# Performance work log

Measured on AMD Instinct MI355X. Metric: run time of the kernel, lower is better.

## Reference

```python
import jax, jax.numpy as jnp
import numpy as np

TEMP = 0.07
HARD_K = 512
EMB_D = 768
PROJ_D = 128
QUEUE = 32768
BATCH = 2048
NUM_CLASSES = 2


def setup_inputs() -> dict:
    key = jax.random.key(0)
    ks = jax.random.split(key, 8)
    embeddings = jax.random.normal(ks[0], (BATCH, EMB_D), dtype=jnp.float32)
    labels = jax.random.randint(ks[1], (BATCH,), 0, NUM_CLASSES)
    # projector params: Linear(D,D) -> ReLU -> Linear(D,128)
    W1 = jax.random.normal(ks[2], (EMB_D, EMB_D), dtype=jnp.float32) * 0.02
    b1 = jnp.zeros((EMB_D,), dtype=jnp.float32)
    W2 = jax.random.normal(ks[3], (EMB_D, PROJ_D), dtype=jnp.float32) * 0.02
    b2 = jnp.zeros((PROJ_D,), dtype=jnp.float32)
    # queue buffers: L2-normalized random embeddings (as in __init__) with valid labels
    qe = jax.random.normal(ks[4], (QUEUE, PROJ_D), dtype=jnp.float32)
    queue_embeddings = qe / jnp.linalg.norm(qe, axis=1, keepdims=True)
    queue_labels = jax.random.randint(ks[5], (QUEUE,), 0, NUM_CLASSES)
    return {
        'embeddings': embeddings, 'labels': labels,
        'W1': W1, 'b1': b1, 'W2': W2, 'b2': b2,
        'queue_embeddings': queue_embeddings, 'queue_labels': queue_labels,
    }


def reference(embeddings, labels, W1, b1, W2, b2, queue_embeddings, queue_labels):
    n = embeddings.shape[0]
    # projector + L2 normalize
    h = jax.nn.relu(embeddings @ W1 + b1)
    z = h @ W2 + b2
    z = z / jnp.linalg.norm(z, axis=1, keepdims=True)  # (N, 128)

    # pairwise in-batch similarities, scaled by temperature
    S = (z @ z.T) / TEMP  # (N, N)
    same = labels[:, None] == labels[None, :]
    eye = jnp.eye(n, dtype=bool)
    pos_mask = same & ~eye           # positives: same label, not self
    neg_mask = ~same                 # in-batch negatives: different label

    # logsumexp over in-batch negatives per anchor (-inf rows -> -inf, handled by logaddexp)
    neg_batch = jnp.where(neg_mask, S, -jnp.inf)
    lse_batch = jax.scipy.special.logsumexp(neg_batch, axis=1)  # (N,)

    # hard negatives from queue: opposite-label, top-K by similarity
    sims_q = z @ queue_embeddings.T  # (N, Q)
    opp = (queue_labels[None, :] != labels[:, None]) & (queue_labels[None, :] >= 0)
    masked_q = jnp.where(opp, sims_q, -jnp.inf)
    topk_vals, _ = jax.lax.top_k(masked_q, HARD_K)  # (N, K); -inf pads drop from logsumexp
    # fallback (no opposite-label entries): first K queue embeddings regardless of label
    fallback = sims_q[:, :HARD_K]
    has_opp = opp.any(axis=1, keepdims=True)
    neg_q = jnp.where(has_opp, topk_vals, fallback) / TEMP
    lse_queue = jax.scipy.special.logsumexp(neg_q, axis=1)  # (N,)

    # all negatives for anchor i: batch negatives ++ queue hard negatives
    lse_neg = jnp.logaddexp(lse_batch, lse_queue)  # (N,)

    # per positive pair (i, j): log_prob = pos_sim - logsumexp([pos_sim, negs])
    log_prob = S - jnp.logaddexp(S, lse_neg[:, None])  # (N, N)
    losses = jnp.where(pos_mask, -log_prob, 0.0)
    count = pos_mask.sum()
    return jnp.where(count > 0, losses.sum() / count.astype(losses.dtype), 0.0)
```

## Files before the change

### kernel.cpp

```cpp
#include <hip/hip_runtime.h>
#include <hip/hip_fp16.h>

#define BATCH_N   2048
#define EMB_D_    768
#define PROJ_D_   128
#define QUEUE_N   32768
#define HARD_K_   512
static constexpr float INV_T  = 1.0f / 0.07f;
static constexpr float WLO    = 0.12f;
static constexpr float S8ENC  = 255.0f / 0.88f;
static constexpr float BINW   = 0.88f / 255.0f;

typedef __attribute__((ext_vector_type(8))) short short8;
typedef __attribute__((ext_vector_type(4))) short short4v;
typedef __attribute__((ext_vector_type(4))) float f32x4;

__device__ __forceinline__ unsigned short f2bf(float f) {
    unsigned u = __float_as_uint(f);
    unsigned r = u + 0x7fffu + ((u >> 16) & 1u);
    return (unsigned short)(r >> 16);
}
__device__ __forceinline__ float bf2f(short s) {
    return __uint_as_float(((unsigned)(unsigned short)s) << 16);
}
__device__ __forceinline__ int opp_of(int mylab, const int* __restrict__ qcnt) {
    const int same = (mylab == 0) ? qcnt[0] : ((mylab == 1) ? qcnt[1] : 0);
    return qcnt[2] - same;
}

__global__ void __launch_bounds__(256) mfma_s_pack(const short* __restrict__ Ab,
                                                   const short* __restrict__ Bb,
                                                   short* __restrict__ C, int N) {
    __shared__ __align__(16) short As[128 * 128];
    __shared__ __align__(16) short Bs[128 * 128];
    const int t = threadIdx.x;
    const int lane = t & 63, wv = t >> 6;
    const int l16 = lane & 15, l4 = lane >> 4;
    const int m0 = blockIdx.y * 128, n0 = blockIdx.x * 128;

    #pragma unroll
    for (int it = 0; it < 8; ++it) {
        const int r = it * 4 + wv, row = r * 4 + l4, cg = l16 ^ (row & 15);
        __builtin_amdgcn_global_load_lds(
            (const __attribute__((address_space(1))) void*)(Ab + (size_t)(m0 + row) * 128 + cg * 8),
            (__attribute__((address_space(3))) void*)(As + r * 512), 16, 0, 0);
    }
    #pragma unroll
    for (int it = 0; it < 8; ++it) {
        const int r = it * 4 + wv, row = r * 4 + l4, cg = l16 ^ (row & 15);
        __builtin_amdgcn_global_load_lds(
            (const __attribute__((address_space(1))) void*)(Bb + (size_t)(n0 + row) * 128 + cg * 8),
            (__attribute__((address_space(3))) void*)(Bs + r * 512), 16, 0, 0);
    }
    __syncthreads();

    const int wm = (wv & 1) * 64, wn = (wv >> 1) * 64;
    f32x4 acc[4][4];
    #pragma unroll
    for (int i = 0; i < 4; ++i)
        #pragma unroll
        for (int j = 0; j < 4; ++j) acc[i][j] = f32x4{0.f, 0.f, 0.f, 0.f};

    #pragma unroll
    for (int ks = 0; ks < 4; ++ks) {
        short8 af[4], bfr[4];
        const int ch = (ks * 4 + l4) ^ l16;
        #pragma unroll
        for (int i = 0; i < 4; ++i) {
            af[i]  = *(const short8*)(As + (wm + i * 16 + l16) * 128 + ch * 8);
            bfr[i] = *(const short8*)(Bs + (wn + i * 16 + l16) * 128 + ch * 8);
        }
        #pragma unroll
        for (int i = 0; i < 4; ++i)
            #pragma unroll
            for (int j = 0; j < 4; ++j)
                acc[i][j] = __builtin_amdgcn_mfma_f32_16x16x32_bf16(af[i], bfr[j], acc[i][j], 0, 0, 0);
    }
    #pragma unroll
    for (int i = 0; i < 4; ++i)
        #pragma unroll
        for (int r = 0; r < 4; ++r) {
            const int m = m0 + wm + i * 16 + l4 * 4 + r;
            union { unsigned short u[4]; uint2 d; } pk;
            #pragma unroll
            for (int j = 0; j < 4; ++j) pk.u[j] = f2bf(acc[i][j][r]);
            *(uint2*)(C + (size_t)m * N + n0 + wn + l16 * 4) = pk.d;
        }
}

__global__ void __launch_bounds__(256) mfma_mask8(const short* __restrict__ Ab,
                                                  const short* __restrict__ Bb,
                                                  unsigned char* __restrict__ codes,
                                                  const int* __restrict__ labA,
                                                  const int* __restrict__ labB) {
    __shared__ __align__(16) short As[128 * 128];
    __shared__ __align__(16) short Bs[128 * 128];
    const int t = threadIdx.x;
    const int lane = t & 63, wv = t >> 6;
    const int l16 = lane & 15, l4 = lane >> 4;
    const int m0 = blockIdx.y * 128;
    const int wm = (wv & 1) * 64, wn = (wv >> 1) * 64;

    #pragma unroll
    for (int it = 0; it < 8; ++it) {
        const int r = it * 4 + wv, row = r * 4 + l4, cg = l16 ^ (row & 15);
        __builtin_amdgcn_global_load_lds(
            (const __attribute__((address_space(1))) void*)(Ab + (size_t)(m0 + row) * 128 + cg * 8),
            (__attribute__((address_space(3))) void*)(As + r * 512), 16, 0, 0);
    }
    {
        const int n0 = (blockIdx.x * 2) * 128;
        #pragma unroll
        for (int it = 0; it < 8; ++it) {
            const int r = it * 4 + wv, row = r * 4 + l4, cg = l16 ^ (row & 15);
            __builtin_amdgcn_global_load_lds(
                (const __attribute__((address_space(1))) void*)(Bb + (size_t)(n0 + row) * 128 + cg * 8),
                (__attribute__((address_space(3))) void*)(Bs + r * 512), 16, 0, 0);
        }
    }

    int la[16];
    #pragma unroll
    for (int i = 0; i < 4; ++i)
        #pragma unroll
        for (int r = 0; r < 4; ++r)
            la[i * 4 + r] = labA[m0 + wm + i * 16 + l4 * 4 + r];
    const float C0 = 1.0f - WLO * S8ENC;
    __syncthreads();

    #pragma unroll
    for (int tt = 0; tt < 2; ++tt) {
        const int n0 = (blockIdx.x * 2 + tt) * 128;

        f32x4 acc[4][4];
        #pragma unroll
        for (int i = 0; i < 4; ++i)
            #pragma unroll
            for (int j = 0; j < 4; ++j) acc[i][j] = f32x4{0.f, 0.f, 0.f, 0.f};

        #pragma unroll
        for (int ks = 0; ks < 4; ++ks) {
            short8 af[4], bfr[4];
            const int ch = (ks * 4 + l4) ^ l16;
            #pragma unroll
            for (int i = 0; i < 4; ++i) {
                af[i]  = *(const short8*)(As + (wm + i * 16 + l16) * 128 + ch * 8);
                bfr[i] = *(const short8*)(Bs + (wn + i * 16 + l16) * 128 + ch * 8);
            }
            #pragma unroll
            for (int i = 0; i < 4; ++i)
                #pragma unroll
                for (int j = 0; j < 4; ++j)
                    acc[i][j] = __builtin_amdgcn_mfma_f32_16x16x32_bf16(af[i], bfr[j], acc[i][j], 0, 0, 0);
        }

        if (tt == 0) {
            __syncthreads();
            const int n1 = (blockIdx.x * 2 + 1) * 128;
            #pragma unroll
            for (int it = 0; it < 8; ++it) {
                const int r = it * 4 + wv, row = r * 4 + l4, cg = l16 ^ (row & 15);
                __builtin_amdgcn_global_load_lds(
                    (const __attribute__((address_space(1))) void*)(Bb + (size_t)(n1 + row) * 128 + cg * 8),
                    (__attribute__((address_space(3))) void*)(Bs + r * 512), 16, 0, 0);
            }
        }

        float a0[4], a1[4];
        #pragma unroll
        for (int j = 0; j < 4; ++j) {
            const int q = labB[n0 + wn + j * 16 + l16];
            a0[j] = (q >= 0 && q != 0) ? C0 : -1e9f;
            a1[j] = (q >= 0 && q != 1) ? C0 : -1e9f;
        }
        #pragma unroll
        for (int i = 0; i < 4; ++i) {
            #pragma unroll
            for (int r = 0; r < 4; ++r) {
                const int m  = m0 + wm + i * 16 + l4 * 4 + r;
                const bool z = (la[i * 4 + r] == 0);
                unsigned pk = 0;
                #pragma unroll
                for (int j = 0; j < 4; ++j) {
                    const float add = z ? a0[j] : a1[j];
                    const float f = fmaf(acc[i][j][r], S8ENC, add);
#if __has_builtin(__builtin_amdgcn_cvt_pk_u8_f32)
                    pk = __builtin_amdgcn_cvt_pk_u8_f32(f, j, pk);
#else
                    const unsigned c = (unsigned)fminf(fmaxf(f, 0.0f), 255.0f);
                    pk |= c << (8 * j);
#endif
                }
                *(unsigned*)(codes + (size_t)m * QUEUE_N + n0 + wn + l16 * 4) = pk;
            }
        }
        if (tt == 0) __syncthreads();
    }
}

template<typename OutT, bool RELU>
__global__ void __launch_bounds__(256) mfma_nt_k(const short* __restrict__ Ab,
                                                 const short* __restrict__ Bb,
                                                 const float* __restrict__ bias,
                                                 OutT* __restrict__ C,
                                                 int N, int K) {
    __shared__ __align__(16) short As[128 * 128];
    __shared__ __align__(16) short Bs[128 * 128];
    const int t = threadIdx.x;
    const int lane = t & 63, wv = t >> 6;
    const int l16 = lane & 15, l4 = lane >> 4;
    const int m0 = blockIdx.y * 128, n0 = blockIdx.x * 128;
    const int wm = (wv & 1) * 64, wn = (wv >> 1) * 64;

    f32x4 acc[4][4];
    #pragma unroll
    for (int i = 0; i < 4; ++i)
        #pragma unroll
        for (int j = 0; j < 4; ++j) acc[i][j] = f32x4{0.f, 0.f, 0.f, 0.f};

    for (int kb = 0; kb < K; kb += 128) {
        __syncthreads();
        #pragma unroll
        for (int it = 0; it < 8; ++it) {
            const int r = it * 4 + wv, row = r * 4 + l4, cg = l16 ^ (row & 15);
            __builtin_amdgcn_global_load_lds(
                (const __attribute__((address_space(1))) void*)(Ab + (size_t)(m0 + row) * K + kb + cg * 8),
                (__attribute__((address_space(3))) void*)(As + r * 512), 16, 0, 0);
        }
        #pragma unroll
        for (int it = 0; it < 8; ++it) {
            const int r = it * 4 + wv, row = r * 4 + l4, cg = l16 ^ (row & 15);
            __builtin_amdgcn_global_load_lds(
                (const __attribute__((address_space(1))) void*)(Bb + (size_t)(n0 + row) * K + kb + cg * 8),
                (__attribute__((address_space(3))) void*)(Bs + r * 512), 16, 0, 0);
        }
        __syncthreads();
        #pragma unroll
        for (int ks = 0; ks < 4; ++ks) {
            short8 af[4], bfr[4];
            const int ch = (ks * 4 + l4) ^ l16;
            #pragma unroll
            for (int i = 0; i < 4; ++i) {
                af[i]  = *(const short8*)(As + (wm + i * 16 + l16) * 128 + ch * 8);
                bfr[i] = *(const short8*)(Bs + (wn + i * 16 + l16) * 128 + ch * 8);
            }
            #pragma unroll
            for (int i = 0; i < 4; ++i)
                #pragma unroll
                for (int j = 0; j < 4; ++j)
                    acc[i][j] = __builtin_amdgcn_mfma_f32_16x16x32_bf16(af[i], bfr[j], acc[i][j], 0, 0, 0);
        }
    }

    float bsv[4];
    #pragma unroll
    for (int j = 0; j < 4; ++j) bsv[j] = bias[n0 + wn + j * 16 + l16];
    #pragma unroll
    for (int i = 0; i < 4; ++i)
        #pragma unroll
        for (int r = 0; r < 4; ++r) {
            const int m = m0 + wm + i * 16 + l4 * 4 + r;
            #pragma unroll
            for (int j = 0; j < 4; ++j) {
                const int n = n0 + wn + j * 16 + l16;
                float v = acc[i][j][r] + bsv[j];
                if (RELU) v = fmaxf(v, 0.0f);
                if constexpr (sizeof(OutT) == 2) ((short*)C)[(size_t)m * N + n] = (short)f2bf(v);
                else                             ((float*)C)[(size_t)m * N + n] = v;
            }
        }
}

__global__ void __launch_bounds__(256) mfma_z_norm(const short* __restrict__ Ab,
                                                   const short* __restrict__ Bb,
                                                   const float* __restrict__ bias,
                                                   short* __restrict__ zb) {
    __shared__ __align__(16) short As[128 * 128];
    __shared__ __align__(16) short Bs[128 * 128];
    __shared__ float ssq[128];
    const int t = threadIdx.x;
    const int lane = t & 63, wv = t >> 6;
    const int l16 = lane & 15, l4 = lane >> 4;
    const int m0 = blockIdx.x * 128;
    const int wm = (wv & 1) * 64, wn = (wv >> 1) * 64;
    const int K = EMB_D_;

    if (t < 128) ssq[t] = 0.0f;

    f32x4 acc[4][4];
    #pragma unroll
    for (int i = 0; i < 4; ++i)
        #pragma unroll
        for (int j = 0; j < 4; ++j) acc[i][j] = f32x4{0.f, 0.f, 0.f, 0.f};

    for (int kb = 0; kb < K; kb += 128) {
        __syncthreads();
        #pragma unroll
        for (int it = 0; it < 8; ++it) {
            const int r = it * 4 + wv, row = r * 4 + l4, cg = l16 ^ (row & 15);
            __builtin_amdgcn_global_load_lds(
                (const __attribute__((address_space(1))) void*)(Ab + (size_t)(m0 + row) * K + kb + cg * 8),
                (__attribute__((address_space(3))) void*)(As + r * 512), 16, 0, 0);
        }
        #pragma unroll
        for (int it = 0; it < 8; ++it) {
            const int r = it * 4 + wv, row = r * 4 + l4, cg = l16 ^ (row & 15);
            __builtin_amdgcn_global_load_lds(
                (const __attribute__((address_space(1))) void*)(Bb + (size_t)(row) * K + kb + cg * 8),
                (__attribute__((address_space(3))) void*)(Bs + r * 512), 16, 0, 0);
        }
        __syncthreads();
        #pragma unroll
        for (int ks = 0; ks < 4; ++ks) {
            short8 af[4], bfr[4];
            const int ch = (ks * 4 + l4) ^ l16;
            #pragma unroll
            for (int i = 0; i < 4; ++i) {
                af[i]  = *(const short8*)(As + (wm + i * 16 + l16) * 128 + ch * 8);
                bfr[i] = *(const short8*)(Bs + (wn + i * 16 + l16) * 128 + ch * 8);
            }
            #pragma unroll
            for (int i = 0; i < 4; ++i)
                #pragma unroll
                for (int j = 0; j < 4; ++j)
                    acc[i][j] = __builtin_amdgcn_mfma_f32_16x16x32_bf16(af[i], bfr[j], acc[i][j], 0, 0, 0);
        }
    }

    float bsv[4];
    #pragma unroll
    for (int j = 0; j < 4; ++j) bsv[j] = bias[wn + j * 16 + l16];
    #pragma unroll
    for (int i = 0; i < 4; ++i)
        #pragma unroll
        for (int r = 0; r < 4; ++r) {
            float p = 0.0f;
            #pragma unroll
            for (int j = 0; j < 4; ++j) {
                acc[i][j][r] += bsv[j];
                p += acc[i][j][r] * acc[i][j][r];
            }
            #pragma unroll
            for (int o = 8; o > 0; o >>= 1) p += __shfl_xor(p, o);
            if (l16 == 0) atomicAdd(&ssq[wm + i * 16 + l4 * 4 + r], p);
        }
    __syncthreads();
    #pragma unroll
    for (int i = 0; i < 4; ++i)
        #pragma unroll
        for (int r = 0; r < 4; ++r) {
            const int lrow = wm + i * 16 + l4 * 4 + r;
            const float inv = rsqrtf(ssq[lrow]);
            #pragma unroll
            for (int j = 0; j < 4; ++j)
                zb[(size_t)(m0 + lrow) * PROJ_D_ + wn + j * 16 + l16] =
                    (short)f2bf(acc[i][j][r] * inv);
        }
}

__global__ void __launch_bounds__(256) prep(const float* __restrict__ emb, short* __restrict__ embb,
                                            const float* __restrict__ queue, short* __restrict__ qb,
                                            const int* __restrict__ qlab, int* __restrict__ qcnt,
                                            const float* __restrict__ W1, short* __restrict__ w1t,
                                            const float* __restrict__ W2, short* __restrict__ w2t) {
    __shared__ float tile[64][65];
    const int b = blockIdx.x, t = threadIdx.x;
    if (b < 1536) {
        const int i = b * 256 + t;
        const float4 f = ((const float4*)emb)[i];
        short4v o = {(short)f2bf(f.x), (short)f2bf(f.y), (short)f2bf(f.z), (short)f2bf(f.w)};
        ((short4v*)embb)[i] = o;
    } else if (b < 5632) {
        const int i = (b - 1536) * 256 + t;
        const float4 f = ((const float4*)queue)[i];
        short4v o = {(short)f2bf(f.x), (short)f2bf(f.y), (short)f2bf(f.z), (short)f2bf(f.w)};
        ((short4v*)qb)[i] = o;
    } else if (b < 5664) {
        const int i = (b - 5632) * 256 + t;
        int c0 = 0, c1 = 0, cv = 0;
        for (int j = i; j < QUEUE_N; j += 8192) {
            const int q = qlab[j];
            c0 += (q == 0); c1 += (q == 1); cv += (q >= 0);
        }
        #pragma unroll
        for (int o = 32; o > 0; o >>= 1) {
            c0 += __shfl_xor(c0, o); c1 += __shfl_xor(c1, o); cv += __shfl_xor(cv, o);
        }
        if ((t & 63) == 0) {
            atomicAdd(&qcnt[0], c0); atomicAdd(&qcnt[1], c1); atomicAdd(&qcnt[2], cv);
        }
    } else {
        const int bid = b - 5664;
        const float* A; short* At; int R, C, bx, by;
        if (bid < 144) { A = W1; At = w1t; R = EMB_D_; C = EMB_D_;  bx = (bid % 12) * 64; by = (bid / 12) * 64; }
        else { const int b2 = bid - 144; A = W2; At = w2t; R = EMB_D_; C = PROJ_D_; bx = (b2 & 1) * 64; by = (b2 >> 1) * 64; }
        const int tc = t & 63, tg = t >> 6;
        #pragma unroll
        for (int i = 0; i < 16; i++) {
            const int r = tg * 16 + i;
            tile[r][tc] = A[(size_t)(by + r) * C + bx + tc];
        }
        __syncthreads();
        #pragma unroll
        for (int i = 0; i < 16; i++) {
            const int r = tg * 16 + i;
            At[(size_t)(bx + r) * R + by + tc] = (short)f2bf(tile[tc][r]);
        }
    }
}

__global__ void __launch_bounds__(256) topk_lse_u8(const unsigned char* __restrict__ codes,
                                                   const int* __restrict__ qcnt,
                                                   const int* __restrict__ labels,
                                                   float* __restrict__ lseq,
                                                   int* __restrict__ flag) {
    const int row = blockIdx.x, t = threadIdx.x;
    __shared__ int hist[256];
    __shared__ int suf[256];
    __shared__ int s_bin;
    __shared__ float scf[4];
    hist[t] = 0;
    __syncthreads();

    const uint4* rowp = (const uint4*)(codes + (size_t)row * QUEUE_N);
    #pragma unroll
    for (int k = 0; k < 8; k++) {
        const uint4 u = rowp[k * 256 + t];
        const unsigned w[4] = {u.x, u.y, u.z, u.w};
        #pragma unroll
        for (int q = 0; q < 4; q++)
            #pragma unroll
            for (int s = 0; s < 4; s++) {
                const int c = (w[q] >> (8 * s)) & 0xFF;
                if (c) atomicAdd(&hist[c], 1);
            }
    }
    __syncthreads();

    suf[t] = hist[t];
    __syncthreads();
    for (int off = 1; off < 256; off <<= 1) {
        int add = (t + off < 256) ? suf[t + off] : 0;
        __syncthreads();
        suf[t] += add;
        __syncthreads();
    }
    const int total = suf[1];
    const int opp   = opp_of(labels[row], qcnt);
    if (total < HARD_K_ || opp < HARD_K_) {
        if (t == 0) flag[row] = 0;
        return;
    }
    {
        const int above = (t < 255) ? suf[t + 1] : 0;
        if (suf[t] >= HARD_K_ && above < HARD_K_) s_bin = t;
    }
    __syncthreads();
    const int b = s_bin;

    float e = 0.0f;
    if (t > b && hist[t]) e = (float)hist[t] * __expf((WLO + ((float)t - 0.5f) * BINW - 1.0f) * INV_T);
    #pragma unroll
    for (int o = 32; o > 0; o >>= 1) e += __shfl_xor(e, o);
    if ((t & 63) == 0) scf[t >> 6] = e;
    __syncthreads();
    if (t == 0) {
        const float Eab  = scf[0] + scf[1] + scf[2] + scf[3];
        const int   cab  = (b < 255) ? suf[b + 1] : 0;
        const float ebin = __expf((WLO + ((float)b - 0.5f) * BINW - 1.0f) * INV_T);
        const float sadj = Eab + (float)(HARD_K_ - cab) * ebin;
        lseq[row] = INV_T + __logf(sadj);
        flag[row] = 1;
    }
}

__device__ __forceinline__ void find_crossing(int* hist, int* grp, int target,
                                              int* s_bin, int* s_chi) {
    const int t = threadIdx.x;
    const int b0 = hist[4*t], b1 = hist[4*t+1], b2 = hist[4*t+2], b3 = hist[4*t+3];
    grp[t] = b0 + b1 + b2 + b3;
    __syncthreads();
    for (int off = 1; off < 256; off <<= 1) {
        int add = (t + off < 256) ? grp[t + off] : 0;
        __syncthreads();
        grp[t] += add;
        __syncthreads();
    }
    int cab = (t < 255) ? grp[t + 1] : 0;
    const int hb[4] = {b0, b1, b2, b3};
    #pragma unroll
    for (int i = 3; i >= 0; i--) {
        const int h = hb[i];
        if (cab < target && cab + h >= target) { *s_bin = 4*t + i; *s_chi = cab; }
        cab += h;
    }
    __syncthreads();
}

#define FOR_ALL_VALS(BODY)                                                   \
    _Pragma("unroll")                                                        \
    for (int _k = 0; _k < 64; _k++) {                                        \
        const float2 _f = __half22float2(*(const __half2*)&dv[_k]);          \
        { const float v = _f.x; BODY }                                       \
        { const float v = _f.y; BODY }                                       \
    }

__global__ void __launch_bounds__(256) topk_lse_fallback(const short* __restrict__ zb,
                                                         const short* __restrict__ qb,
                                                         const int* __restrict__ labels,
                                                         const int* __restrict__ qlab,
                                                         const int* __restrict__ qcnt,
                                                         const int* __restrict__ flag,
                                                         float* __restrict__ lseq) {
    const int row = blockIdx.x, t = threadIdx.x;
    if (flag[row]) return;
    const int opp = opp_of(labels[row], qcnt);

    __shared__ float zrow[128];
    __shared__ int hist[1024];
    __shared__ int grp[256];
    __shared__ int s_bin, s_chi, s_bin2, s_chi2;
    __shared__ float scf[4]; __shared__ int sci[4];
    if (t < 128) zrow[t] = bf2f(zb[(size_t)row * 128 + t]);
    __syncthreads();

    const int mylab = labels[row];
    unsigned dv[64];
    float rm = -1e30f, rs = 0.0f;
    for (int k = 0; k < 128; k++) {
        const int j = t + 256 * k;
        float d = 0.0f;
        #pragma unroll
        for (int c = 0; c < 16; ++c) {
            const short8 qv = *(const short8*)(qb + (size_t)j * 128 + c * 8);
            #pragma unroll
            for (int e = 0; e < 8; ++e) d += zrow[c * 8 + e] * bf2f(qv[e]);
        }
        if (j < HARD_K_) {
            const float sv = d * INV_T;
            if (sv > rm) { rs = rs * __expf(rm - sv) + 1.0f; rm = sv; }
            else         { rs += __expf(sv - rm); }
        }
        const int q = qlab[j];
        const float mv = (q != mylab && q >= 0) ? d : -65504.0f;
        const __half h = __float2half(mv);
        unsigned short* p = (unsigned short*)&dv[k >> 1];
        p[k & 1] = *(const unsigned short*)&h;
    }

    if (opp == 0) {
        #pragma unroll
        for (int o = 32; o > 0; o >>= 1) {
            const float om = __shfl_xor(rm, o), os = __shfl_xor(rs, o);
            const float nm = fmaxf(rm, om);
            rs = rs * __expf(rm - nm) + os * __expf(om - nm);
            rm = nm;
        }
        if ((t & 63) == 0) { scf[t >> 6] = rm; ((float*)sci)[t >> 6] = rs; }
        __syncthreads();
        if (t == 0) {
            float M = -1e30f, Sx = 0.0f;
            for (int w = 0; w < 4; w++) {
                const float nm = fmaxf(M, scf[w]);
                Sx = Sx * __expf(M - nm) + ((float*)sci)[w] * __expf(scf[w] - nm);
                M = nm;
            }
            lseq[row] = M + __logf(Sx);
        }
        return;
    }
    if (opp < HARD_K_) {
        float mm = -1e30f, ss = 0.0f;
        FOR_ALL_VALS(
            if (v > -60000.0f) {
                const float sv = v * INV_T;
                if (sv > mm) { ss = ss * __expf(mm - sv) + 1.0f; mm = sv; }
                else         { ss += __expf(sv - mm); }
            } )
        #pragma unroll
        for (int o = 32; o > 0; o >>= 1) {
            const float om = __shfl_xor(mm, o), os = __shfl_xor(ss, o);
            const float nm = fmaxf(mm, om);
            ss = ss * __expf(mm - nm) + os * __expf(om - nm);
            mm = nm;
        }
        if ((t & 63) == 0) { scf[t >> 6] = mm; ((float*)sci)[t >> 6] = ss; }
        __syncthreads();
        if (t == 0) {
            float M = -1e30f, Sx = 0.0f;
            for (int w = 0; w < 4; w++) {
                const float nm = fmaxf(M, scf[w]);
                Sx = Sx * __expf(M - nm) + ((float*)sci)[w] * __expf(scf[w] - nm);
                M = nm;
            }
            lseq[row] = M + __logf(Sx);
        }
        return;
    }

    float mloc = -1e30f;
    FOR_ALL_VALS( mloc = fmaxf(mloc, v); )
    #pragma unroll
    for (int o = 32; o > 0; o >>= 1) mloc = fmaxf(mloc, __shfl_xor(mloc, o));
    if ((t & 63) == 0) scf[t >> 6] = mloc;
    __syncthreads();
    const float m = fmaxf(fmaxf(scf[0], scf[1]), fmaxf(scf[2], scf[3]));

    int c1 = 0, c2 = 0;
    const float w1 = m - 0.25f, w2 = m - 1.0f;
    FOR_ALL_VALS( c1 += (v >= w1); c2 += (v >= w2); )
    #pragma unroll
    for (int o = 32; o > 0; o >>= 1) { c1 += __shfl_xor(c1, o); c2 += __shfl_xor(c2, o); }
    if ((t & 63) == 0) { sci[t >> 6] = c1; }
    __syncthreads();
    const int C1 = sci[0] + sci[1] + sci[2] + sci[3];
    __syncthreads();
    if ((t & 63) == 0) { sci[t >> 6] = c2; }
    __syncthreads();
    const int C2 = sci[0] + sci[1] + sci[2] + sci[3];

    float lo;
    if      (C1 >= HARD_K_) lo = w1;
    else if (C2 >= HARD_K_) lo = w2;
    else                    lo = -1.01f;
    const float range = m - lo;
    const float scale = 1024.0f / range;

    for (int k = t; k < 1024; k += 256) hist[k] = 0;
    __syncthreads();
    FOR_ALL_VALS(
        if (v >= lo) {
            const float bf = fminf((v - lo) * scale, 1023.0f);
            atomicAdd(&hist[(int)bf], 1);
        } )
    __syncthreads();
    find_crossing(hist, grp, HARD_K_, &s_bin, &s_chi);
    const int   bin1 = s_bin, chi1 = s_chi;
    const float binw = range * (1.0f / 1024.0f);
    const float lo1  = lo + bin1 * binw;
    const float ssc  = 1024.0f / binw;

    for (int k = t; k < 1024; k += 256) hist[k] = 0;
    __syncthreads();
    FOR_ALL_VALS(
        if (v >= lo) {
            const float bf = fminf((v - lo) * scale, 1023.0f);
            if ((int)bf == bin1) {
                const float sf = fminf(fmaxf((v - lo1) * ssc, 0.0f), 1023.0f);
                atomicAdd(&hist[(int)sf], 1);
            }
        } )
    __syncthreads();
    find_crossing(hist, grp, HARD_K_ - chi1, &s_bin2, &s_chi2);
    const float thr = lo1 + s_bin2 * (binw * (1.0f / 1024.0f));

    float sl = 0.0f; int cg = 0;
    FOR_ALL_VALS( if (v > thr) { cg++; sl += __expf((v - m) * INV_T); } )
    #pragma unroll
    for (int o = 32; o > 0; o >>= 1) { sl += __shfl_xor(sl, o); cg += __shfl_xor(cg, o); }
    if ((t & 63) == 0) { scf[t >> 6] = sl; sci[t >> 6] = cg; }
    __syncthreads();
    if (t == 0) {
        const float slt = scf[0] + scf[1] + scf[2] + scf[3];
        const int   cgt = sci[0] + sci[1] + sci[2] + sci[3];
        const float sadj = slt + ((float)HARD_K_ - (float)cgt) * __expf((thr - m) * INV_T);
        lseq[row] = m * INV_T + __logf(sadj);
    }
}

__global__ void __launch_bounds__(256) batch_row_loss(const short* __restrict__ S,
                                                      const int* __restrict__ labels,
                                                      const float* __restrict__ lse_queue,
                                                      float* __restrict__ part_out,
                                                      int* __restrict__ cnt_out) {
    const int t = threadIdx.x;
    const int wv = t >> 6, lane = t & 63;
    const int row = blockIdx.x * 4 + wv;
    __shared__ int plab[BATCH_N];
    for (int idx = t; idx < BATCH_N; idx += 256) {
        const int col = (idx & ~63) + ((idx & 3) << 4) + ((idx >> 2) & 15);
        plab[idx] = labels[col];
    }
    __syncthreads();
    const int myLab = labels[row];
    const uint4* rp = (const uint4*)(S + (size_t)row * BATCH_N);

    float v[32]; int lb[32];
    #pragma unroll
    for (int kk = 0; kk < 4; kk++) {
        const uint4 u = rp[lane + 64 * kk];
        const unsigned w[4] = {u.x, u.y, u.z, u.w};
        const int base = (lane + 64 * kk) * 8;
        #pragma unroll
        for (int q = 0; q < 4; q++) {
            v[kk * 8 + 2 * q]     = __uint_as_float(w[q] << 16);
            v[kk * 8 + 2 * q + 1] = __uint_as_float(w[q] & 0xFFFF0000u);
            lb[kk * 8 + 2 * q]     = plab[base + 2 * q];
            lb[kk * 8 + 2 * q + 1] = plab[base + 2 * q + 1];
        }
    }

    const float REF = INV_T;
    float sneg = 0.0f;
    #pragma unroll
    for (int k = 0; k < 32; k++) {
        const float ev = __expf(v[k] * INV_T - REF);
        sneg += (lb[k] != myLab) ? ev : 0.0f;
    }
    #pragma unroll
    for (int o = 32; o > 0; o >>= 1) sneg += __shfl_xor(sneg, o);
    const float lseb = (sneg > 0.0f) ? REF + __logf(sneg) : -1e30f;
    const float Lq = lse_queue[row];
    const float mx0 = fmaxf(lseb, Lq), mn0 = fminf(lseb, Lq);
    const float L = mx0 + __logf(1.0f + __expf(mn0 - mx0));

    float part = 0.0f; int cnt = 0;
    #pragma unroll
    for (int k = 0; k < 32; k++) {
        const int idx = ((lane + 64 * (k >> 3)) * 8) + (k & 7);
        const int col = (idx & ~63) + ((idx & 3) << 4) + ((idx >> 2) & 15);
        if (lb[k] == myLab && col != row) {
            const float sv = v[k] * INV_T;
            const float mx = fmaxf(sv, L), mn = fminf(sv, L);
            part += (mx - sv) + __logf(1.0f + __expf(mn - mx));
            cnt++;
        }
    }
    #pragma unroll
    for (int o = 32; o > 0; o >>= 1) { part += __shfl_xor(part, o); cnt += __shfl_xor(cnt, o); }
    if (lane == 0) { part_out[row] = part; cnt_out[row] = cnt; }
}

__global__ void __launch_bounds__(256) finalize_loss(const float* __restrict__ part,
                                                     const int* __restrict__ cnt,
                                                     float* __restrict__ out) {
    const int t = threadIdx.x;
    float s = 0.0f; int c = 0;
    #pragma unroll
    for (int k = 0; k < 8; k++) { s += part[t + 256 * k]; c += cnt[t + 256 * k]; }
    #pragma unroll
    for (int o = 32; o > 0; o >>= 1) { s += __shfl_xor(s, o); c += __shfl_xor(c, o); }
    __shared__ float sf[4]; __shared__ int sc[4];
    if ((t & 63) == 0) { sf[t >> 6] = s; sc[t >> 6] = c; }
    __syncthreads();
    if (t == 0) {
        const float st = sf[0] + sf[1] + sf[2] + sf[3];
        const int   ct = sc[0] + sc[1] + sc[2] + sc[3];
        out[0] = (ct > 0) ? (st / (float)ct) : 0.0f;
    }
}

extern "C" void kernel_launch(void* const* d_in, const int* in_sizes, int n_in,
                              void* d_out, int out_size, void* d_ws, size_t ws_size,
                              hipStream_t stream) {
    const float* emb    = (const float*)d_in[0];
    const int*   labels = (const int*)  d_in[1];
    const float* W1     = (const float*)d_in[2];
    const float* b1     = (const float*)d_in[3];
    const float* W2     = (const float*)d_in[4];
    const float* b2     = (const float*)d_in[5];
    const float* queue  = (const float*)d_in[6];
    const int*   qlab   = (const int*)  d_in[7];

    char* ws = (char*)d_ws;
    short*         Sbuf  = (short*)        (ws);
    unsigned char* codes = (unsigned char*)(ws + 16777216);
    short*         embb  = (short*)        (ws + 83886080);
    short*         hbf   = (short*)        (ws + 87031808);
    short*         zb    = (short*)        (ws + 90177536);
    short*         qb    = (short*)        (ws + 90701824);
    short*         w1t   = (short*)        (ws + 99090432);
    short*         w2t   = (short*)        (ws + 100270080);
    float*         lseq  = (float*)        (ws + 100466688);
    int*           flag  = (int*)          (ws + 100474880);
    int*           qcnt  = (int*)          (ws + 100483072);
    float*         partb = (float*)        (ws + 100483136);
    int*           cntb  = (int*)          (ws + 100491328);

    hipMemsetAsync(ws + 100474880, 0, 8192 + 64, stream);

    dim3 blk(256);
    prep<<<dim3(5832), blk, 0, stream>>>(emb, embb, queue, qb, qlab, qcnt, W1, w1t, W2, w2t);
    mfma_nt_k<short, true><<<dim3(EMB_D_ / 128, BATCH_N / 128), blk, 0, stream>>>(embb, w1t, b1, hbf, EMB_D_, EMB_D_);
    mfma_z_norm<<<dim3(BATCH_N / 128), blk, 0, stream>>>(hbf, w2t, b2, zb);
    mfma_mask8<<<dim3(QUEUE_N / 256, BATCH_N / 128), blk, 0, stream>>>(zb, qb, codes, labels, qlab);
    topk_lse_u8<<<BATCH_N, blk, 0, stream>>>(codes, qcnt, labels, lseq, flag);
    topk_lse_fallback<<<BATCH_N, blk, 0, stream>>>(zb, qb, labels, qlab, qcnt, flag, lseq);
    mfma_s_pack<<<dim3(BATCH_N / 128, BATCH_N / 128), blk, 0, stream>>>(zb, zb, Sbuf, BATCH_N);
    batch_row_loss<<<BATCH_N / 4, blk, 0, stream>>>(Sbuf, labels, lseq, partb, cntb);
    finalize_loss<<<1, blk, 0, stream>>>(partb, cntb, (float*)d_out);
}
```

Measured before the change: 177.0 us.

## Use 64-row tiles for projector GEMMs and widen mask8 per-block queue span

The two projector GEMMs (h and z-normalize) switch from 128x128 to 64-row tiles, with each wave covering 32 columns. This doubles the number of blocks so more CUs are busy on these small GEMMs. The queue-similarity mask kernel now processes four 128-column queue tiles per block instead of two, reusing the loaded A tile across more work and halving its grid. The trade-off is more blocks with less reuse on the projector GEMMs, and longer serial per-block work with fewer blocks in mask8.

```diff
diff --git a/kernel.cpp b/kernel.cpp
--- a/kernel.cpp
+++ b/kernel.cpp
@@ -109,7 +109,7 @@
             (__attribute__((address_space(3))) void*)(As + r * 512), 16, 0, 0);
     }
     {
-        const int n0 = (blockIdx.x * 2) * 128;
+        const int n0 = (blockIdx.x * 4) * 128;
         #pragma unroll
         for (int it = 0; it < 8; ++it) {
             const int r = it * 4 + wv, row = r * 4 + l4, cg = l16 ^ (row & 15);
@@ -129,8 +129,8 @@
     __syncthreads();
 
     #pragma unroll
-    for (int tt = 0; tt < 2; ++tt) {
-        const int n0 = (blockIdx.x * 2 + tt) * 128;
+    for (int tt = 0; tt < 4; ++tt) {
+        const int n0 = (blockIdx.x * 4 + tt) * 128;
 
         f32x4 acc[4][4];
         #pragma unroll
@@ -154,9 +154,9 @@
                     acc[i][j] = __builtin_amdgcn_mfma_f32_16x16x32_bf16(af[i], bfr[j], acc[i][j], 0, 0, 0);
         }
 
-        if (tt == 0) {
+        if (tt < 3) {
             __syncthreads();
-            const int n1 = (blockIdx.x * 2 + 1) * 128;
+            const int n1 = (blockIdx.x * 4 + tt + 1) * 128;
             #pragma unroll
             for (int it = 0; it < 8; ++it) {
                 const int r = it * 4 + wv, row = r * 4 + l4, cg = l16 ^ (row & 15);
@@ -194,34 +194,33 @@
                 *(unsigned*)(codes + (size_t)m * QUEUE_N + n0 + wn + l16 * 4) = pk;
             }
         }
-        if (tt == 0) __syncthreads();
-    }
-}
-
-template<typename OutT, bool RELU>
-__global__ void __launch_bounds__(256) mfma_nt_k(const short* __restrict__ Ab,
-                                                 const short* __restrict__ Bb,
-                                                 const float* __restrict__ bias,
-                                                 OutT* __restrict__ C,
-                                                 int N, int K) {
-    __shared__ __align__(16) short As[128 * 128];
+        if (tt < 3) __syncthreads();
+    }
+}
+
+__global__ void __launch_bounds__(256) mfma_h64(const short* __restrict__ Ab,
+                                                const short* __restrict__ Bb,
+                                                const float* __restrict__ bias,
+                                                short* __restrict__ C,
+                                                int N, int K) {
+    __shared__ __align__(16) short As[64 * 128];
     __shared__ __align__(16) short Bs[128 * 128];
     const int t = threadIdx.x;
     const int lane = t & 63, wv = t >> 6;
     const int l16 = lane & 15, l4 = lane >> 4;
-    const int m0 = blockIdx.y * 128, n0 = blockIdx.x * 128;
-    const int wm = (wv & 1) * 64, wn = (wv >> 1) * 64;
-
-    f32x4 acc[4][4];
+    const int m0 = blockIdx.y * 64, n0 = blockIdx.x * 128;
+    const int wn = wv * 32;
+
+    f32x4 acc[4][2];
     #pragma unroll
     for (int i = 0; i < 4; ++i)
         #pragma unroll
-        for (int j = 0; j < 4; ++j) acc[i][j] = f32x4{0.f, 0.f, 0.f, 0.f};
+        for (int j = 0; j < 2; ++j) acc[i][j] = f32x4{0.f, 0.f, 0.f, 0.f};
 
     for (int kb = 0; kb < K; kb += 128) {
         __syncthreads();
         #pragma unroll
-        for (int it = 0; it < 8; ++it) {
+        for (int it = 0; it < 4; ++it) {
             const int r = it * 4 + wv, row = r * 4 + l4, cg = l16 ^ (row & 15);
             __builtin_amdgcn_global_load_lds(
                 (const __attribute__((address_space(1))) void*)(Ab + (size_t)(m0 + row) * K + kb + cg * 8),
@@ -237,66 +236,65 @@
         __syncthreads();
         #pragma unroll
         for (int ks = 0; ks < 4; ++ks) {
-            short8 af[4], bfr[4];
+            short8 af[4], bfr[2];
             const int ch = (ks * 4 + l4) ^ l16;
             #pragma unroll
-            for (int i = 0; i < 4; ++i) {
-                af[i]  = *(const short8*)(As + (wm + i * 16 + l16) * 128 + ch * 8);
-                bfr[i] = *(const short8*)(Bs + (wn + i * 16 + l16) * 128 + ch * 8);
-            }
+            for (int i = 0; i < 4; ++i)
+                af[i] = *(const short8*)(As + (i * 16 + l16) * 128 + ch * 8);
+            #pragma unroll
+            for (int j = 0; j < 2; ++j)
+                bfr[j] = *(const short8*)(Bs + (wn + j * 16 + l16) * 128 + ch * 8);
             #pragma unroll
             for (int i = 0; i < 4; ++i)
                 #pragma unroll
-                for (int j = 0; j < 4; ++j)
+                for (int j = 0; j < 2; ++j)
                     acc[i][j] = __builtin_amdgcn_mfma_f32_16x16x32_bf16(af[i], bfr[j], acc[i][j], 0, 0, 0);
         }
     }
 
-    float bsv[4];
-    #pragma unroll
-    for (int j = 0; j < 4; ++j) bsv[j] = bias[n0 + wn + j * 16 + l16];
+    float bsv[2];
+    #pragma unroll
+    for (int j = 0; j < 2; ++j) bsv[j] = bias[n0 + wn + j * 16 + l16];
     #pragma unroll
     for (int i = 0; i < 4; ++i)
         #pragma unroll
         for (int r = 0; r < 4; ++r) {
-            const int m = m0 + wm + i * 16 + l4 * 4 + r;
-            #pragma unroll
-            for (int j = 0; j < 4; ++j) {
+            const int m = m0 + i * 16 + l4 * 4 + r;
+            #pragma unroll
+            for (int j = 0; j < 2; ++j) {
                 const int n = n0 + wn + j * 16 + l16;
-                float v = acc[i][j][r] + bsv[j];
-                if (RELU) v = fmaxf(v, 0.0f);
-                if constexpr (sizeof(OutT) == 2) ((short*)C)[(size_t)m * N + n] = (short)f2bf(v);
-                else                             ((float*)C)[(size_t)m * N + n] = v;
-            }
-        }
-}
-
-__global__ void __launch_bounds__(256) mfma_z_norm(const short* __restrict__ Ab,
-                                                   const short* __restrict__ Bb,
-                                                   const float* __restrict__ bias,
-                                                   short* __restrict__ zb) {
-    __shared__ __align__(16) short As[128 * 128];
+                const float v = fmaxf(acc[i][j][r] + bsv[j], 0.0f);
+                C[(size_t)m * N + n] = (short)f2bf(v);
+            }
+        }
+}
+
+__global__ void __launch_bounds__(256) mfma_z_norm64(const short* __restrict__ Ab,
+                                                     const short* __restrict__ Bb,
+                                                     const float* __restrict__ bias,
+                                                     short* __restrict__ zb) {
+    __shared__ __align__(16) short As[64 * 128];
     __shared__ __align__(16) short Bs[128 * 128];
-    __shared__ float ssq[128];
+    __shared__ float ssq[64];
     const int t = threadIdx.x;
     const int lane = t & 63, wv = t >> 6;
     const int l16 = lane & 15, l4 = lane >> 4;
-    const int m0 = blockIdx.x * 128;
-    const int wm = (wv & 1) * 64, wn = (wv >> 1) * 64;
+    const int m0 = blockIdx.x * 64;
+    const int wn = wv * 32;
     const int K = EMB_D_;
 
-    if (t < 128) ssq[t] = 0.0f;
-
-    f32x4 acc[4][4];
+    if (t < 64) ssq[t] = 0.0f;
+
+    f32x4 acc[4][2];
     #pragma unroll
     for (int i = 0; i < 4; ++i)
         #pragma unroll
-        for (int j = 0; j < 4; ++j) acc[i][j] = f32x4{0.f, 0.f, 0.f, 0.f};
+        for (int j = 0; j < 2; ++j) acc[i][j] = f32x4{0.f, 0.f, 0.f, 0.f};
 
     for (int kb = 0; kb < K; kb += 128) {
         __syncthreads();
         #pragma unroll
-        for (int it = 0; it < 8; ++it) {
+        for (int it = 0; it < 4; ++it) {
             const int r = it * 4 + wv, row = r * 4 + l4, cg = l16 ^ (row & 15);
             __builtin_amdgcn_global_load_lds(
                 (const __attribute__((address_space(1))) void*)(Ab + (size_t)(m0 + row) * K + kb + cg * 8),
@@ -312,47 +310,48 @@
         __syncthreads();
         #pragma unroll
         for (int ks = 0; ks < 4; ++ks) {
-            short8 af[4], bfr[4];
+            short8 af[4], bfr[2];
             const int ch = (ks * 4 + l4) ^ l16;
             #pragma unroll
-            for (int i = 0; i < 4; ++i) {
-                af[i]  = *(const short8*)(As + (wm + i * 16 + l16) * 128 + ch * 8);
-                bfr[i] = *(const short8*)(Bs + (wn + i * 16 + l16) * 128 + ch * 8);
-            }
+            for (int i = 0; i < 4; ++i)
+                af[i] = *(const short8*)(As + (i * 16 + l16) * 128 + ch * 8);
+            #pragma unroll
+            for (int j = 0; j < 2; ++j)
+                bfr[j] = *(const short8*)(Bs + (wn + j * 16 + l16) * 128 + ch * 8);
             #pragma unroll
             for (int i = 0; i < 4; ++i)
                 #pragma unroll
-                for (int j = 0; j < 4; ++j)
+                for (int j = 0; j < 2; ++j)
                     acc[i][j] = __builtin_amdgcn_mfma_f32_16x16x32_bf16(af[i], bfr[j], acc[i][j], 0, 0, 0);
         }
     }
 
-    float bsv[4];
-    #pragma unroll
-    for (int j = 0; j < 4; ++j) bsv[j] = bias[wn + j * 16 + l16];
+    float bsv[2];
+    #pragma unroll
+    for (int j = 0; j < 2; ++j) bsv[j] = bias[wn + j * 16 + l16];
     #pragma unroll
     for (int i = 0; i < 4; ++i)
         #pragma unroll
         for (int r = 0; r < 4; ++r) {
             float p = 0.0f;
             #pragma unroll
-            for (int j = 0; j < 4; ++j) {
+            for (int j = 0; j < 2; ++j) {
                 acc[i][j][r] += bsv[j];
                 p += acc[i][j][r] * acc[i][j][r];
             }
             #pragma unroll
             for (int o = 8; o > 0; o >>= 1) p += __shfl_xor(p, o);
-            if (l16 == 0) atomicAdd(&ssq[wm + i * 16 + l4 * 4 + r], p);
+            if (l16 == 0) atomicAdd(&ssq[i * 16 + l4 * 4 + r], p);
         }
     __syncthreads();
     #pragma unroll
     for (int i = 0; i < 4; ++i)
         #pragma unroll
         for (int r = 0; r < 4; ++r) {
-            const int lrow = wm + i * 16 + l4 * 4 + r;
+            const int lrow = i * 16 + l4 * 4 + r;
             const float inv = rsqrtf(ssq[lrow]);
             #pragma unroll
-            for (int j = 0; j < 4; ++j)
+            for (int j = 0; j < 2; ++j)
                 zb[(size_t)(m0 + lrow) * PROJ_D_ + wn + j * 16 + l16] =
                     (short)f2bf(acc[i][j][r] * inv);
         }
@@ -781,9 +780,9 @@
 
     dim3 blk(256);
     prep<<<dim3(5832), blk, 0, stream>>>(emb, embb, queue, qb, qlab, qcnt, W1, w1t, W2, w2t);
-    mfma_nt_k<short, true><<<dim3(EMB_D_ / 128, BATCH_N / 128), blk, 0, stream>>>(embb, w1t, b1, hbf, EMB_D_, EMB_D_);
-    mfma_z_norm<<<dim3(BATCH_N / 128), blk, 0, stream>>>(hbf, w2t, b2, zb);
-    mfma_mask8<<<dim3(QUEUE_N / 256, BATCH_N / 128), blk, 0, stream>>>(zb, qb, codes, labels, qlab);
+    mfma_h64<<<dim3(EMB_D_ / 128, BATCH_N / 64), blk, 0, stream>>>(embb, w1t, b1, hbf, EMB_D_, EMB_D_);
+    mfma_z_norm64<<<dim3(BATCH_N / 64), blk, 0, stream>>>(hbf, w2t, b2, zb);
+    mfma_mask8<<<dim3(QUEUE_N / 512, BATCH_N / 128), blk, 0, stream>>>(zb, qb, codes, labels, qlab);
     topk_lse_u8<<<BATCH_N, blk, 0, stream>>>(codes, qcnt, labels, lseq, flag);
     topk_lse_fallback<<<BATCH_N, blk, 0, stream>>>(zb, qb, labels, qlab, qcnt, flag, lseq);
     mfma_s_pack<<<dim3(BATCH_N / 128, BATCH_N / 128), blk, 0, stream>>>(zb, zb, Sbuf, BATCH_N);
```

Measured after the change: 167.1 us. -5.6%, faster.
